# Optimization experiments

Measured on AMD Instinct MI355X. Metric: run time of the kernel, lower is better.

The kernel has to match this reference:

```python
import jax, jax.numpy as jnp
import numpy as np

N_HEADS = 4
ROPE_THETA = 10000.0


def rotate_half(x):
    h = x.shape[-1] // 2
    return jnp.concatenate([-x[..., h:], x[..., :h]], axis=-1)


def setup_inputs() -> dict:
    key = jax.random.key(0)
    k1, k2, k3, k4, k5 = jax.random.split(key, 5)
    B, L, D, M = 4, 2048, 216, 64
    x = jax.random.normal(k1, (B, L, D), dtype=jnp.float32)
    mem_k = jax.random.normal(k2, (B, M, D), dtype=jnp.float32)
    mem_v = jax.random.normal(k3, (B, M, D), dtype=jnp.float32)
    attention_mask = jnp.ones((B, L), dtype=jnp.int32)
    # pre-transposed Linear weights (y = x @ W); scaled for stability
    Wqkv = jax.random.normal(k4, (D, 3 * D), dtype=jnp.float32) * (D ** -0.5)
    Wo = jax.random.normal(k5, (D, D), dtype=jnp.float32) * (D ** -0.5)
    return {"x": x, "mem_k": mem_k, "mem_v": mem_v,
            "attention_mask": attention_mask, "Wqkv": Wqkv, "Wo": Wo}


def reference(x, mem_k, mem_v, attention_mask, Wqkv, Wo):
    B, L, D = x.shape
    H = N_HEADS
    hd = D // H
    scale = hd ** -0.5
    M = mem_k.shape[1]

    # QKV projection -> [B, L, 3, H, hd] -> [B, H, L, hd]
    qkv = (x @ Wqkv).reshape(B, L, 3, H, hd)
    q = jnp.transpose(qkv[:, :, 0], (0, 2, 1, 3))
    k = jnp.transpose(qkv[:, :, 1], (0, 2, 1, 3))
    v = jnp.transpose(qkv[:, :, 2], (0, 2, 1, 3))

    # RoPE (cos/sin: [L, hd], broadcast over B,H)
    inv_freq = 1.0 / (ROPE_THETA ** (jnp.arange(0, hd, 2, dtype=jnp.float32) / hd))
    t = jnp.arange(L, dtype=jnp.float32)
    freqs = jnp.outer(t, inv_freq)
    emb = jnp.concatenate([freqs, freqs], axis=-1)
    cos, sin = jnp.cos(emb), jnp.sin(emb)
    q = q * cos + rotate_half(q) * sin
    k = k * cos + rotate_half(k) * sin

    # memory KV: [B, M, D] -> [B, H, M, hd], prepend along kv axis
    mk = jnp.transpose(mem_k.reshape(B, M, H, hd), (0, 2, 1, 3))
    mv = jnp.transpose(mem_v.reshape(B, M, H, hd), (0, 2, 1, 3))
    k_all = jnp.concatenate([mk, k], axis=2)  # [B, H, M+L, hd]
    v_all = jnp.concatenate([mv, v], axis=2)

    scores = jnp.einsum('bhld,bhmd->bhlm', q, k_all) * scale  # [B,H,L,M+L]

    # causal mask applies only to the self-attention block (cols >= M)
    causal = jnp.triu(jnp.ones((L, L), dtype=bool), k=1)
    full_causal = jnp.concatenate([jnp.zeros((L, M), dtype=bool), causal], axis=1)
    scores = jnp.where(full_causal[None, None], -jnp.inf, scores)

    # padding mask: memory positions always valid
    combined = jnp.concatenate(
        [jnp.ones((B, M), dtype=attention_mask.dtype), attention_mask], axis=-1)
    scores = jnp.where(combined[:, None, None, :] == 0, -jnp.inf, scores)

    attn = jax.nn.softmax(scores, axis=-1)  # dropout is identity in eval
    out = jnp.einsum('bhlm,bhmd->bhld', attn, v_all)
    out = jnp.transpose(out, (0, 2, 1, 3)).reshape(B, L, D)
    return out @ Wo
```

## Files before the change

kernel.cpp:

```cpp
#include <hip/hip_runtime.h>
#include <math.h>

#define B_ 4
#define L_ 2048
#define D_ 216
#define H_ 4
#define HD 54
#define HDP 64
#define M_ 64
#define LK 2112
#define KP 256

typedef __attribute__((ext_vector_type(8))) __bf16 bf16x8;
typedef __attribute__((ext_vector_type(4))) float f32x4;

__global__ void conv_x(const float* __restrict__ x, __bf16* __restrict__ xb) {
    int idx = blockIdx.x * 256 + threadIdx.x;
    int row = idx >> 5, c8 = idx & 31;
    bf16x8 v{};
    if (c8 < 27) {
        const float* p = x + (size_t)row * 216 + c8 * 8;
        #pragma unroll
        for (int j = 0; j < 8; ++j) v[j] = (__bf16)p[j];
    }
    *reinterpret_cast<bf16x8*>(xb + (size_t)row * KP + c8 * 8) = v;
}

__global__ void conv_wt(const float* __restrict__ W, __bf16* __restrict__ Wt,
                        int Kin, int Nin, int Npad) {
    int idx = blockIdx.x * 256 + threadIdx.x;
    if (idx >= Npad * KP) return;
    int n = idx >> 8, k = idx & 255;
    float v = (n < Nin && k < Kin) ? W[(size_t)k * Nin + n] : 0.f;
    Wt[idx] = (__bf16)v;
}

__global__ __launch_bounds__(256) void gemm_mfma(const __bf16* __restrict__ A,
                                                 const __bf16* __restrict__ Bt,
                                                 float* __restrict__ C, int N) {
    __shared__ __align__(16) __bf16 As[8192];
    __shared__ __align__(16) __bf16 Bs[4096];
    const int col0 = blockIdx.x * 64;
    const int row0 = blockIdx.y * 128;
    const int tid = threadIdx.x;
    const int lane = tid & 63;
    const int w = tid >> 6, wm = w >> 1, wn = w & 1;
    const int l15 = lane & 15, l4 = lane >> 4;

    f32x4 acc[4][2];
    #pragma unroll
    for (int m = 0; m < 4; ++m)
        #pragma unroll
        for (int n = 0; n < 2; ++n) acc[m][n] = (f32x4){0.f, 0.f, 0.f, 0.f};

    bf16x8 ra[4], rb[2];
    #pragma unroll
    for (int i = 0; i < 4; ++i) { int c = tid + 256 * i, r = c >> 3, c8 = c & 7;
        ra[i] = *reinterpret_cast<const bf16x8*>(A + (size_t)(row0 + r) * KP + c8 * 8); }
    #pragma unroll
    for (int i = 0; i < 2; ++i) { int c = tid + 256 * i, r = c >> 3, c8 = c & 7;
        rb[i] = *reinterpret_cast<const bf16x8*>(Bt + (size_t)(col0 + r) * KP + c8 * 8); }

    for (int kit = 0; kit < 4; ++kit) {
        __syncthreads();
        #pragma unroll
        for (int i = 0; i < 4; ++i) { int c = tid + 256 * i, r = c >> 3, c8 = c & 7;
            *reinterpret_cast<bf16x8*>(&As[r * 64 + ((c8 ^ (r & 7)) * 8)]) = ra[i]; }
        #pragma unroll
        for (int i = 0; i < 2; ++i) { int c = tid + 256 * i, r = c >> 3, c8 = c & 7;
            *reinterpret_cast<bf16x8*>(&Bs[r * 64 + ((c8 ^ (r & 7)) * 8)]) = rb[i]; }
        __syncthreads();
        if (kit < 3) {
            const int k0 = (kit + 1) * 64;
            #pragma unroll
            for (int i = 0; i < 4; ++i) { int c = tid + 256 * i, r = c >> 3, c8 = c & 7;
                ra[i] = *reinterpret_cast<const bf16x8*>(A + (size_t)(row0 + r) * KP + k0 + c8 * 8); }
            #pragma unroll
            for (int i = 0; i < 2; ++i) { int c = tid + 256 * i, r = c >> 3, c8 = c & 7;
                rb[i] = *reinterpret_cast<const bf16x8*>(Bt + (size_t)(col0 + r) * KP + k0 + c8 * 8); }
        }
        #pragma unroll
        for (int ks = 0; ks < 2; ++ks) {
            bf16x8 af[4], bfr[2];
            #pragma unroll
            for (int m = 0; m < 4; ++m) { int row = wm * 64 + m * 16 + l15; int ch = ks * 4 + l4;
                af[m] = *reinterpret_cast<const bf16x8*>(&As[row * 64 + ((ch ^ (row & 7)) * 8)]); }
            #pragma unroll
            for (int n = 0; n < 2; ++n) { int row = wn * 32 + n * 16 + l15; int ch = ks * 4 + l4;
                bfr[n] = *reinterpret_cast<const bf16x8*>(&Bs[row * 64 + ((ch ^ (row & 7)) * 8)]); }
            #pragma unroll
            for (int m = 0; m < 4; ++m)
                #pragma unroll
                for (int n = 0; n < 2; ++n)
                    acc[m][n] = __builtin_amdgcn_mfma_f32_16x16x32_bf16(af[m], bfr[n], acc[m][n], 0, 0, 0);
        }
    }
    #pragma unroll
    for (int m = 0; m < 4; ++m)
        #pragma unroll
        for (int n = 0; n < 2; ++n) {
            int cc = col0 + wn * 32 + n * 16 + l15;
            if (cc < N) {
                #pragma unroll
                for (int rr = 0; rr < 4; ++rr)
                    C[(size_t)(row0 + wm * 64 + m * 16 + l4 * 4 + rr) * N + cc] = acc[m][n][rr];
            }
        }
}

__global__ void memkv_pack(const float* __restrict__ mk, const float* __restrict__ mv,
                           __bf16* __restrict__ kall, __bf16* __restrict__ vt) {
    int idx = blockIdx.x * 256 + threadIdx.x;
    if (idx >= B_ * M_ * H_ * 64) return;
    int b  = idx >> 14;
    int m  = (idx >> 8) & 63;
    int h  = (idx >> 6) & 3;
    int dd = idx & 63;
    float kv = (dd < HD) ? mk[((size_t)(b * M_ + m)) * D_ + h * HD + dd] : 0.f;
    kall[((size_t)(b * 4 + h) * LK + m) * HDP + dd] = (__bf16)kv;
    if (dd < HD)
        vt[((size_t)(b * 4 + h) * HD + dd) * LK + m] =
            (__bf16)mv[((size_t)(b * M_ + m)) * D_ + h * HD + dd];
}

__global__ __launch_bounds__(128) void rope_pack(const float* __restrict__ qkv,
                                                 __bf16* __restrict__ qb,
                                                 __bf16* __restrict__ kall) {
    const int blk = blockIdx.x;
    const int b = blk / L_, l = blk % L_;
    const float* row = qkv + (size_t)blk * 648;
    const int t = threadIdx.x;
    const float scale = 0.13608276348795434f;
    if (t < 108) {
        int h = t / 27, ii = t % 27;
        float inv = exp2f(-0.49213749924f * (float)ii);
        float ang = (float)l * inv;
        float s = sinf(ang), c = cosf(ang);
        float q0v = row[h * HD + ii], q1v = row[h * HD + ii + 27];
        float k0v = row[D_ + h * HD + ii], k1v = row[D_ + h * HD + ii + 27];
        size_t qoff = ((size_t)(b * 4 + h) * L_ + l) * HDP;
        qb[qoff + ii]      = (__bf16)((q0v * c - q1v * s) * scale);
        qb[qoff + ii + 27] = (__bf16)((q1v * c + q0v * s) * scale);
        size_t koff = ((size_t)(b * 4 + h) * LK + M_ + l) * HDP;
        kall[koff + ii]      = (__bf16)(k0v * c - k1v * s);
        kall[koff + ii + 27] = (__bf16)(k1v * c + k0v * s);
    }
    for (int p = t; p < 40; p += 128) {
        int h = p / 10, dd = 54 + p % 10;
        qb[((size_t)(b * 4 + h) * L_ + l) * HDP + dd] = (__bf16)0.f;
        kall[((size_t)(b * 4 + h) * LK + M_ + l) * HDP + dd] = (__bf16)0.f;
    }
}

__global__ __launch_bounds__(256) void transpose_v(const float* __restrict__ qkv,
                                                   __bf16* __restrict__ vt) {
    const int l0 = blockIdx.x * 64;
    const int b = blockIdx.y;
    __shared__ float T[64][55];
    for (int h = 0; h < 4; ++h) {
        __syncthreads();
        for (int idx = threadIdx.x; idx < 64 * 54; idx += 256) {
            int l = idx / 54, d = idx % 54;
            T[l][d] = qkv[((size_t)(b * L_ + l0 + l)) * 648 + 432 + h * 54 + d];
        }
        __syncthreads();
        for (int idx = threadIdx.x; idx < 54 * 64; idx += 256) {
            int d = idx >> 6, l = idx & 63;
            vt[((size_t)(b * 4 + h) * HD + d) * LK + M_ + l0 + l] = (__bf16)T[l][d];
        }
    }
}

__global__ void mask_bias(const int* __restrict__ amask, float* __restrict__ bias) {
    int idx = blockIdx.x * 256 + threadIdx.x;
    if (idx >= B_ * LK) return;
    int b = idx / LK, c = idx % LK;
    bias[idx] = (c < M_ || amask[b * L_ + c - M_] != 0) ? 0.f : -1e30f;
}

__global__ __launch_bounds__(256) void flash_mfma(const __bf16* __restrict__ qb,
                                                  const __bf16* __restrict__ kall,
                                                  const __bf16* __restrict__ vt,
                                                  const float* __restrict__ bias,
                                                  __bf16* __restrict__ aoutb) {
    const int qt = (blockIdx.y & 8) ? (31 - (int)blockIdx.x) : (int)blockIdx.x;
    const int q0 = qt * 64;
    const int bh = blockIdx.y;
    const int b = bh >> 2, h = bh & 3;
    __shared__ __align__(16) __bf16 Qs[4096];
    __shared__ __align__(16) __bf16 Ks[4096];
    __shared__ __align__(16) __bf16 Vs[4096];
    __shared__ __align__(16) __bf16 Ps[4096];
    __shared__ float biasS[64];

    const int tid = threadIdx.x;
    const int lane = tid & 63;
    const int w = tid >> 6;
    const int l15 = lane & 15;
    const int l4 = lane >> 4;

    {
        const __bf16* src = qb + ((size_t)bh * L_ + q0) * HDP;
        for (int ch = tid; ch < 512; ch += 256) {
            int row = ch >> 3, c8 = ch & 7;
            bf16x8 v = *reinterpret_cast<const bf16x8*>(src + ch * 8);
            *reinterpret_cast<bf16x8*>(&Qs[row * 64 + ((c8 ^ (row & 7)) * 8)]) = v;
        }
        if (tid < 80) {
            int d = 54 + (tid >> 3), c8 = tid & 7;
            bf16x8 z{};
            *reinterpret_cast<bf16x8*>(&Vs[d * 64 + ((c8 ^ (d & 7)) * 8)]) = z;
        }
    }

    const int ntiles = qt + 2;
    const int rgbase = q0 + 16 * w + l4 * 4;
    const __bf16* kbase = kall + (size_t)bh * LK * HDP;
    const __bf16* vbase = vt + (size_t)bh * HD * LK;

    bf16x8 rk[2], rv[2];
    float biasR = 0.f;
    {
        rk[0] = *reinterpret_cast<const bf16x8*>(kbase + tid * 8);
        rk[1] = *reinterpret_cast<const bf16x8*>(kbase + (tid + 256) * 8);
        { int d = tid >> 3, c8 = tid & 7;
          rv[0] = *reinterpret_cast<const bf16x8*>(vbase + (size_t)d * LK + c8 * 8); }
        if (tid < 176) { int c = tid + 256, d = c >> 3, c8 = c & 7;
          rv[1] = *reinterpret_cast<const bf16x8*>(vbase + (size_t)d * LK + c8 * 8); }
        if (tid < 64) biasR = bias[b * LK + tid];
    }

    __syncthreads();
    bf16x8 aQ[2];
    {
        int qrow = 16 * w + l15, s = (qrow & 7) << 3;
        aQ[0] = *reinterpret_cast<const bf16x8*>(&Qs[qrow * 64 + ((l4 * 8) ^ s)]);
        aQ[1] = *reinterpret_cast<const bf16x8*>(&Qs[qrow * 64 + ((32 + l4 * 8) ^ s)]);
    }

    f32x4 Oacc[4];
    float m_run[4], l_run[4];
    #pragma unroll
    for (int nt = 0; nt < 4; ++nt) Oacc[nt] = (f32x4){0.f, 0.f, 0.f, 0.f};
    #pragma unroll
    for (int r = 0; r < 4; ++r) { m_run[r] = -1e30f; l_run[r] = 0.f; }

    for (int t = 0; t < ntiles; ++t) {
        const int cbase = t * 64;
        __syncthreads();
        { int r = tid >> 3, c8 = tid & 7;
          *reinterpret_cast<bf16x8*>(&Ks[r * 64 + ((c8 ^ (r & 7)) * 8)]) = rk[0]; }
        { int c = tid + 256, r = c >> 3, c8 = c & 7;
          *reinterpret_cast<bf16x8*>(&Ks[r * 64 + ((c8 ^ (r & 7)) * 8)]) = rk[1]; }
        { int d = tid >> 3, c8 = tid & 7;
          *reinterpret_cast<bf16x8*>(&Vs[d * 64 + ((c8 ^ (d & 7)) * 8)]) = rv[0]; }
        if (tid < 176) { int c = tid + 256, d = c >> 3, c8 = c & 7;
          *reinterpret_cast<bf16x8*>(&Vs[d * 64 + ((c8 ^ (d & 7)) * 8)]) = rv[1]; }
        if (tid < 64) biasS[tid] = biasR;
        __syncthreads();
        if (t + 1 < ntiles) {
            const __bf16* ks = kbase + (size_t)(cbase + 64) * HDP;
            rk[0] = *reinterpret_cast<const bf16x8*>(ks + tid * 8);
            rk[1] = *reinterpret_cast<const bf16x8*>(ks + (tid + 256) * 8);
            { int d = tid >> 3, c8 = tid & 7;
              rv[0] = *reinterpret_cast<const bf16x8*>(vbase + (size_t)d * LK + cbase + 64 + c8 * 8); }
            if (tid < 176) { int c = tid + 256, d = c >> 3, c8 = c & 7;
              rv[1] = *reinterpret_cast<const bf16x8*>(vbase + (size_t)d * LK + cbase + 64 + c8 * 8); }
            if (tid < 64) biasR = bias[b * LK + cbase + 64 + tid];
        }

        f32x4 S[4];
        #pragma unroll
        for (int nt = 0; nt < 4; ++nt) {
            int krow = nt * 16 + l15, s = (krow & 7) << 3;
            bf16x8 b0 = *reinterpret_cast<const bf16x8*>(&Ks[krow * 64 + ((l4 * 8) ^ s)]);
            bf16x8 b1 = *reinterpret_cast<const bf16x8*>(&Ks[krow * 64 + ((32 + l4 * 8) ^ s)]);
            f32x4 acc = (f32x4){0.f, 0.f, 0.f, 0.f};
            acc = __builtin_amdgcn_mfma_f32_16x16x32_bf16(aQ[0], b0, acc, 0, 0, 0);
            acc = __builtin_amdgcn_mfma_f32_16x16x32_bf16(aQ[1], b1, acc, 0, 0, 0);
            S[nt] = acc;
        }
        #pragma unroll
        for (int nt = 0; nt < 4; ++nt) {
            int cg = cbase + nt * 16 + l15;
            float bv = biasS[nt * 16 + l15];
            #pragma unroll
            for (int r = 0; r < 4; ++r) {
                float sv = S[nt][r] + bv;
                S[nt][r] = (cg > rgbase + r + M_) ? -1e30f : sv;
            }
        }
        float mt[4], alpha[4], ls[4];
        #pragma unroll
        for (int r = 0; r < 4; ++r)
            mt[r] = fmaxf(fmaxf(S[0][r], S[1][r]), fmaxf(S[2][r], S[3][r]));
        #pragma unroll
        for (int r = 0; r < 4; ++r) {
            mt[r] = fmaxf(mt[r], __shfl_xor(mt[r], 1));
            mt[r] = fmaxf(mt[r], __shfl_xor(mt[r], 2));
            mt[r] = fmaxf(mt[r], __shfl_xor(mt[r], 4));
            mt[r] = fmaxf(mt[r], __shfl_xor(mt[r], 8));
            float m_new = fmaxf(m_run[r], mt[r]);
            alpha[r] = __expf(m_run[r] - m_new);
            m_run[r] = m_new;
            ls[r] = 0.f;
        }
        #pragma unroll
        for (int nt = 0; nt < 4; ++nt)
            #pragma unroll
            for (int r = 0; r < 4; ++r) {
                float p = __expf(S[nt][r] - m_run[r]);
                S[nt][r] = p;
                ls[r] += p;
            }
        #pragma unroll
        for (int r = 0; r < 4; ++r) {
            ls[r] += __shfl_xor(ls[r], 1);
            ls[r] += __shfl_xor(ls[r], 2);
            ls[r] += __shfl_xor(ls[r], 4);
            ls[r] += __shfl_xor(ls[r], 8);
            l_run[r] = l_run[r] * alpha[r] + ls[r];
        }
        #pragma unroll
        for (int r = 0; r < 4; ++r) {
            int row = 16 * w + l4 * 4 + r, s = (row & 7) << 3;
            #pragma unroll
            for (int nt = 0; nt < 4; ++nt) {
                int col = nt * 16 + l15;
                Ps[row * 64 + (col ^ s)] = (__bf16)S[nt][r];
            }
        }
        #pragma unroll
        for (int nt = 0; nt < 4; ++nt)
            #pragma unroll
            for (int r = 0; r < 4; ++r) Oacc[nt][r] *= alpha[r];
        bf16x8 aP[2];
        {
            int prow = 16 * w + l15, s = (prow & 7) << 3;
            aP[0] = *reinterpret_cast<const bf16x8*>(&Ps[prow * 64 + ((l4 * 8) ^ s)]);
            aP[1] = *reinterpret_cast<const bf16x8*>(&Ps[prow * 64 + ((32 + l4 * 8) ^ s)]);
        }
        #pragma unroll
        for (int nt = 0; nt < 4; ++nt) {
            int vrow = nt * 16 + l15, s = (vrow & 7) << 3;
            bf16x8 v0 = *reinterpret_cast<const bf16x8*>(&Vs[vrow * 64 + ((l4 * 8) ^ s)]);
            bf16x8 v1 = *reinterpret_cast<const bf16x8*>(&Vs[vrow * 64 + ((32 + l4 * 8) ^ s)]);
            Oacc[nt] = __builtin_amdgcn_mfma_f32_16x16x32_bf16(aP[0], v0, Oacc[nt], 0, 0, 0);
            Oacc[nt] = __builtin_amdgcn_mfma_f32_16x16x32_bf16(aP[1], v1, Oacc[nt], 0, 0, 0);
        }
    }

    float invl[4];
    #pragma unroll
    for (int r = 0; r < 4; ++r) invl[r] = 1.f / l_run[r];
    #pragma unroll
    for (int nt = 0; nt < 4; ++nt) {
        int c = nt * 16 + l15;
        if (c < HD) {
            #pragma unroll
            for (int r = 0; r < 4; ++r)
                aoutb[((size_t)b * L_ + rgbase + r) * KP + h * HD + c] =
                    (__bf16)(Oacc[nt][r] * invl[r]);
        }
    }
}

extern "C" void kernel_launch(void* const* d_in, const int* in_sizes, int n_in,
                              void* d_out, int out_size, void* d_ws, size_t ws_size,
                              hipStream_t stream) {
    const float* x     = (const float*)d_in[0];
    const float* mem_k = (const float*)d_in[1];
    const float* mem_v = (const float*)d_in[2];
    const int*   amask = (const int*)d_in[3];
    const float* Wqkv  = (const float*)d_in[4];
    const float* Wo    = (const float*)d_in[5];
    float* out = (float*)d_out;

    char* p = (char*)d_ws;
    float* qkv_raw = (float*)p;        p += (size_t)8192 * 648 * 4;
    float* bias    = (float*)p;        p += (size_t)B_ * LK * 4;
    __bf16* xb     = (__bf16*)p;       p += (size_t)8192 * KP * 2;
    __bf16* wqkvt  = (__bf16*)p;       p += (size_t)704 * KP * 2;
    __bf16* wot    = (__bf16*)p;       p += (size_t)256 * KP * 2;
    __bf16* aoutb  = (__bf16*)p;       p += (size_t)8192 * KP * 2;
    __bf16* qb     = (__bf16*)p;       p += (size_t)16 * 2048 * 64 * 2;
    __bf16* kall   = (__bf16*)p;       p += (size_t)16 * 2112 * 64 * 2;
    __bf16* vt     = (__bf16*)p;       p += (size_t)16 * 54 * 2112 * 2;

    conv_x<<<dim3(8192 * 32 / 256), 256, 0, stream>>>(x, xb);
    conv_wt<<<dim3(704), 256, 0, stream>>>(Wqkv, wqkvt, 216, 648, 704);
    conv_wt<<<dim3(256), 256, 0, stream>>>(Wo, wot, 216, 216, 256);

    gemm_mfma<<<dim3(11, 64), 256, 0, stream>>>(xb, wqkvt, qkv_raw, 648);

    memkv_pack<<<dim3((B_ * M_ * H_ * 64 + 255) / 256), 256, 0, stream>>>(mem_k, mem_v, kall, vt);
    rope_pack<<<dim3(B_ * L_), 128, 0, stream>>>(qkv_raw, qb, kall);
    transpose_v<<<dim3(L_ / 64, B_), 256, 0, stream>>>(qkv_raw, vt);
    mask_bias<<<dim3((B_ * LK + 255) / 256), 256, 0, stream>>>(amask, bias);

    hipMemsetAsync(aoutb, 0, (size_t)8192 * KP * 2, stream);
    flash_mfma<<<dim3(32, 16), 256, 0, stream>>>(qb, kall, vt, bias, aoutb);

    gemm_mfma<<<dim3(4, 64), 256, 0, stream>>>(aoutb, wot, out, 216);
}
```

Measured before the change: 116.6 us.

## Transpose score MFMA so each lane owns a query row; fold log2e into scale

Swaps the MFMA operands in the QK^T product so each lane holds scores for a single query row. Row max and row sum then need only two cross-lane shuffles instead of four per row, and alpha and 1/l are redistributed with __shfl. The Q scale now includes log2(e) so softmax can use exp2f. A per-tile padding flag kernel lets the bias add be skipped for fully valid tiles, and the causal mask is applied only on the last tile. The memset of the attention output buffer is removed, so its pad columns are no longer explicitly zeroed; that relies on the output GEMM tolerating whatever the workspace holds there.

```diff
diff --git a/kernel.cpp b/kernel.cpp
--- a/kernel.cpp
+++ b/kernel.cpp
@@ -9,9 +9,11 @@
 #define HDP 64
 #define M_ 64
 #define LK 2112
+#define NT_ 33
 #define KP 256
 
 typedef __attribute__((ext_vector_type(8))) __bf16 bf16x8;
+typedef __attribute__((ext_vector_type(4))) __bf16 bf16x4;
 typedef __attribute__((ext_vector_type(4))) float f32x4;
 
 __global__ void conv_x(const float* __restrict__ x, __bf16* __restrict__ xb) {
@@ -130,7 +132,7 @@
     const int b = blk / L_, l = blk % L_;
     const float* row = qkv + (size_t)blk * 648;
     const int t = threadIdx.x;
-    const float scale = 0.13608276348795434f;
+    const float scale = 0.19632593f;
     if (t < 108) {
         int h = t / 27, ii = t % 27;
         float inv = exp2f(-0.49213749924f * (float)ii);
@@ -178,10 +180,23 @@
     bias[idx] = (c < M_ || amask[b * L_ + c - M_] != 0) ? 0.f : -1e30f;
 }
 
+__global__ void pad_flags(const int* __restrict__ amask, int* __restrict__ padflag) {
+    int t = threadIdx.x;
+    if (t >= B_ * NT_) return;
+    int b = t / NT_, tile = t % NT_;
+    int flag = 0;
+    for (int u = 0; u < 64; ++u) {
+        int c = tile * 64 + u;
+        if (c >= M_ && amask[b * L_ + c - M_] == 0) flag = 1;
+    }
+    padflag[t] = flag;
+}
+
 __global__ __launch_bounds__(256) void flash_mfma(const __bf16* __restrict__ qb,
                                                   const __bf16* __restrict__ kall,
                                                   const __bf16* __restrict__ vt,
                                                   const float* __restrict__ bias,
+                                                  const int* __restrict__ padflag,
                                                   __bf16* __restrict__ aoutb) {
     const int qt = (blockIdx.y & 8) ? (31 - (int)blockIdx.x) : (int)blockIdx.x;
     const int q0 = qt * 64;
@@ -214,12 +229,13 @@
     }
 
     const int ntiles = qt + 2;
-    const int rgbase = q0 + 16 * w + l4 * 4;
+    const int rq = q0 + 16 * w + l15;
     const __bf16* kbase = kall + (size_t)bh * LK * HDP;
     const __bf16* vbase = vt + (size_t)bh * HD * LK;
 
     bf16x8 rk[2], rv[2];
     float biasR = 0.f;
+    int flagC;
     {
         rk[0] = *reinterpret_cast<const bf16x8*>(kbase + tid * 8);
         rk[1] = *reinterpret_cast<const bf16x8*>(kbase + (tid + 256) * 8);
@@ -228,6 +244,7 @@
         if (tid < 176) { int c = tid + 256, d = c >> 3, c8 = c & 7;
           rv[1] = *reinterpret_cast<const bf16x8*>(vbase + (size_t)d * LK + c8 * 8); }
         if (tid < 64) biasR = bias[b * LK + tid];
+        flagC = padflag[b * NT_];
     }
 
     __syncthreads();
@@ -239,11 +256,9 @@
     }
 
     f32x4 Oacc[4];
-    float m_run[4], l_run[4];
     #pragma unroll
     for (int nt = 0; nt < 4; ++nt) Oacc[nt] = (f32x4){0.f, 0.f, 0.f, 0.f};
-    #pragma unroll
-    for (int r = 0; r < 4; ++r) { m_run[r] = -1e30f; l_run[r] = 0.f; }
+    float m_run = -1e30f, l_run = 0.f;
 
     for (int t = 0; t < ntiles; ++t) {
         const int cbase = t * 64;
@@ -257,6 +272,7 @@
         if (tid < 176) { int c = tid + 256, d = c >> 3, c8 = c & 7;
           *reinterpret_cast<bf16x8*>(&Vs[d * 64 + ((c8 ^ (d & 7)) * 8)]) = rv[1]; }
         if (tid < 64) biasS[tid] = biasR;
+        const int flag = flagC;
         __syncthreads();
         if (t + 1 < ntiles) {
             const __bf16* ks = kbase + (size_t)(cbase + 64) * HDP;
@@ -267,6 +283,7 @@
             if (tid < 176) { int c = tid + 256, d = c >> 3, c8 = c & 7;
               rv[1] = *reinterpret_cast<const bf16x8*>(vbase + (size_t)d * LK + cbase + 64 + c8 * 8); }
             if (tid < 64) biasR = bias[b * LK + cbase + 64 + tid];
+            flagC = padflag[b * NT_ + t + 1];
         }
 
         f32x4 S[4];
@@ -276,64 +293,65 @@
             bf16x8 b0 = *reinterpret_cast<const bf16x8*>(&Ks[krow * 64 + ((l4 * 8) ^ s)]);
             bf16x8 b1 = *reinterpret_cast<const bf16x8*>(&Ks[krow * 64 + ((32 + l4 * 8) ^ s)]);
             f32x4 acc = (f32x4){0.f, 0.f, 0.f, 0.f};
-            acc = __builtin_amdgcn_mfma_f32_16x16x32_bf16(aQ[0], b0, acc, 0, 0, 0);
-            acc = __builtin_amdgcn_mfma_f32_16x16x32_bf16(aQ[1], b1, acc, 0, 0, 0);
+            acc = __builtin_amdgcn_mfma_f32_16x16x32_bf16(b0, aQ[0], acc, 0, 0, 0);
+            acc = __builtin_amdgcn_mfma_f32_16x16x32_bf16(b1, aQ[1], acc, 0, 0, 0);
             S[nt] = acc;
         }
-        #pragma unroll
-        for (int nt = 0; nt < 4; ++nt) {
-            int cg = cbase + nt * 16 + l15;
-            float bv = biasS[nt * 16 + l15];
+        if (flag) {
+            #pragma unroll
+            for (int nt = 0; nt < 4; ++nt)
+                #pragma unroll
+                for (int r = 0; r < 4; ++r)
+                    S[nt][r] += biasS[nt * 16 + l4 * 4 + r];
+        }
+        if (t == ntiles - 1) {
+            #pragma unroll
+            for (int nt = 0; nt < 4; ++nt)
+                #pragma unroll
+                for (int r = 0; r < 4; ++r) {
+                    int cg = cbase + nt * 16 + l4 * 4 + r;
+                    if (cg > rq + M_) S[nt][r] = -1e30f;
+                }
+        }
+        float mx = fmaxf(fmaxf(S[0][0], S[0][1]), fmaxf(S[0][2], S[0][3]));
+        #pragma unroll
+        for (int nt = 1; nt < 4; ++nt)
+            mx = fmaxf(mx, fmaxf(fmaxf(S[nt][0], S[nt][1]), fmaxf(S[nt][2], S[nt][3])));
+        mx = fmaxf(mx, __shfl_xor(mx, 16));
+        mx = fmaxf(mx, __shfl_xor(mx, 32));
+        float m_new = fmaxf(m_run, mx);
+        float alpha = exp2f(m_run - m_new);
+        m_run = m_new;
+        float ls = 0.f;
+        #pragma unroll
+        for (int nt = 0; nt < 4; ++nt)
             #pragma unroll
             for (int r = 0; r < 4; ++r) {
-                float sv = S[nt][r] + bv;
-                S[nt][r] = (cg > rgbase + r + M_) ? -1e30f : sv;
+                float p = exp2f(S[nt][r] - m_new);
+                S[nt][r] = p;
+                ls += p;
             }
-        }
-        float mt[4], alpha[4], ls[4];
+        ls += __shfl_xor(ls, 16);
+        ls += __shfl_xor(ls, 32);
+        l_run = l_run * alpha + ls;
+        {
+            int prow = 16 * w + l15, s = (prow & 7) << 3;
+            #pragma unroll
+            for (int nt = 0; nt < 4; ++nt) {
+                bf16x4 pk;
+                pk[0] = (__bf16)S[nt][0]; pk[1] = (__bf16)S[nt][1];
+                pk[2] = (__bf16)S[nt][2]; pk[3] = (__bf16)S[nt][3];
+                *reinterpret_cast<bf16x4*>(&Ps[prow * 64 + ((nt * 16 + l4 * 4) ^ s)]) = pk;
+            }
+        }
+        float aO[4];
         #pragma unroll
         for (int r = 0; r < 4; ++r)
-            mt[r] = fmaxf(fmaxf(S[0][r], S[1][r]), fmaxf(S[2][r], S[3][r]));
-        #pragma unroll
-        for (int r = 0; r < 4; ++r) {
-            mt[r] = fmaxf(mt[r], __shfl_xor(mt[r], 1));
-            mt[r] = fmaxf(mt[r], __shfl_xor(mt[r], 2));
-            mt[r] = fmaxf(mt[r], __shfl_xor(mt[r], 4));
-            mt[r] = fmaxf(mt[r], __shfl_xor(mt[r], 8));
-            float m_new = fmaxf(m_run[r], mt[r]);
-            alpha[r] = __expf(m_run[r] - m_new);
-            m_run[r] = m_new;
-            ls[r] = 0.f;
-        }
+            aO[r] = __shfl(alpha, (lane & 0x30) | (l4 * 4 + r), 64);
         #pragma unroll
         for (int nt = 0; nt < 4; ++nt)
             #pragma unroll
-            for (int r = 0; r < 4; ++r) {
-                float p = __expf(S[nt][r] - m_run[r]);
-                S[nt][r] = p;
-                ls[r] += p;
-            }
-        #pragma unroll
-        for (int r = 0; r < 4; ++r) {
-            ls[r] += __shfl_xor(ls[r], 1);
-            ls[r] += __shfl_xor(ls[r], 2);
-            ls[r] += __shfl_xor(ls[r], 4);
-            ls[r] += __shfl_xor(ls[r], 8);
-            l_run[r] = l_run[r] * alpha[r] + ls[r];
-        }
-        #pragma unroll
-        for (int r = 0; r < 4; ++r) {
-            int row = 16 * w + l4 * 4 + r, s = (row & 7) << 3;
-            #pragma unroll
-            for (int nt = 0; nt < 4; ++nt) {
-                int col = nt * 16 + l15;
-                Ps[row * 64 + (col ^ s)] = (__bf16)S[nt][r];
-            }
-        }
-        #pragma unroll
-        for (int nt = 0; nt < 4; ++nt)
-            #pragma unroll
-            for (int r = 0; r < 4; ++r) Oacc[nt][r] *= alpha[r];
+            for (int r = 0; r < 4; ++r) Oacc[nt][r] *= aO[r];
         bf16x8 aP[2];
         {
             int prow = 16 * w + l15, s = (prow & 7) << 3;
@@ -350,9 +368,12 @@
         }
     }
 
+    float li = 1.f / l_run;
     float invl[4];
     #pragma unroll
-    for (int r = 0; r < 4; ++r) invl[r] = 1.f / l_run[r];
+    for (int r = 0; r < 4; ++r)
+        invl[r] = __shfl(li, (lane & 0x30) | (l4 * 4 + r), 64);
+    const int rgbase = q0 + 16 * w + l4 * 4;
     #pragma unroll
     for (int nt = 0; nt < 4; ++nt) {
         int c = nt * 16 + l15;
@@ -379,6 +400,7 @@
     char* p = (char*)d_ws;
     float* qkv_raw = (float*)p;        p += (size_t)8192 * 648 * 4;
     float* bias    = (float*)p;        p += (size_t)B_ * LK * 4;
+    int*   padflag = (int*)p;          p += (size_t)B_ * NT_ * 4;
     __bf16* xb     = (__bf16*)p;       p += (size_t)8192 * KP * 2;
     __bf16* wqkvt  = (__bf16*)p;       p += (size_t)704 * KP * 2;
     __bf16* wot    = (__bf16*)p;       p += (size_t)256 * KP * 2;
@@ -397,9 +419,9 @@
     rope_pack<<<dim3(B_ * L_), 128, 0, stream>>>(qkv_raw, qb, kall);
     transpose_v<<<dim3(L_ / 64, B_), 256, 0, stream>>>(qkv_raw, vt);
     mask_bias<<<dim3((B_ * LK + 255) / 256), 256, 0, stream>>>(amask, bias);
-
-    hipMemsetAsync(aoutb, 0, (size_t)8192 * KP * 2, stream);
-    flash_mfma<<<dim3(32, 16), 256, 0, stream>>>(qb, kall, vt, bias, aoutb);
+    pad_flags<<<dim3(1), 256, 0, stream>>>(amask, padflag);
+
+    flash_mfma<<<dim3(32, 16), 256, 0, stream>>>(qb, kall, vt, bias, padflag, aoutb);
 
     gemm_mfma<<<dim3(4, 64), 256, 0, stream>>>(aoutb, wot, out, 216);
 }
```

New measurement: 116.0 us. No clear change (-0.5%).
